# Kernel optimization log

Measured on AMD Instinct MI355X. Metric: run time of the kernel, lower is better.

Reference implementation:

```python
import jax, jax.numpy as jnp
import numpy as np

N_NODES = 100000
N_EDGES = 1600000
IN_DIM = 48
HID = 128
BN_EPS = 1e-5


def _batchnorm(h, gamma, beta):
    # BatchNorm1d in training mode: batch mean, biased variance
    mu = jnp.mean(h, axis=0)
    var = jnp.mean(jnp.square(h - mu), axis=0)
    return (h - mu) * jax.lax.rsqrt(var + BN_EPS) * gamma + beta


def setup_inputs() -> dict:
    key = jax.random.key(0)
    ks = jax.random.split(key, 8)
    x = jax.random.normal(ks[0], (N_NODES, IN_DIM), dtype=jnp.float32)
    edge_index = jax.random.randint(ks[1], (2, N_EDGES), 0, N_NODES, dtype=jnp.int64)
    s1 = 1.0 / np.sqrt(IN_DIM)
    s2 = 1.0 / np.sqrt(HID)
    return {
        "x": x,
        "edge_index": edge_index,
        "W1": jax.random.uniform(ks[2], (HID, IN_DIM), jnp.float32, -s1, s1),
        "b1": jnp.zeros((HID,), jnp.float32),
        "g1": jnp.ones((HID,), jnp.float32),
        "be1": jnp.zeros((HID,), jnp.float32),
        "Wl": jax.random.uniform(ks[3], (HID, HID), jnp.float32, -s2, s2),
        "bl": jnp.zeros((HID,), jnp.float32),
        "Wr": jax.random.uniform(ks[4], (HID, HID), jnp.float32, -s2, s2),
        "g2": jnp.ones((HID,), jnp.float32),
        "be2": jnp.zeros((HID,), jnp.float32),
    }


def reference(x, edge_index, W1, b1, g1, be1, Wl, bl, Wr, g2, be2):
    # input projection: Linear -> BatchNorm -> ReLU
    h = x @ W1.T + b1                               # [N, HID]
    feat = jax.nn.relu(_batchnorm(h, g1, be1))      # [N, HID]

    # SAGEConv (mean aggregation): messages flow src -> dst
    src, dst = edge_index[0], edge_index[1]
    summed = jax.ops.segment_sum(feat[src], dst, num_segments=N_NODES)  # [N, HID]
    cnt = jax.ops.segment_sum(jnp.ones((N_EDGES,), jnp.float32), dst, num_segments=N_NODES)
    agg = summed / jnp.maximum(cnt, 1.0)[:, None]
    sage = agg @ Wl.T + bl + feat @ Wr.T            # lin_l(mean) + lin_r(self)

    out_feat = _batchnorm(sage, g2, be2)
    return (feat, out_feat)
```

## Files before the change

kernel.cpp:

```cpp
#include <hip/hip_runtime.h>
#include <hip/hip_bf16.h>

#define NN 100000
#define NE 1600000
#define INDIM 48
#define HID 128
#define K2 256
#define KP 64
#define BN_EPS 1e-5f

#define NBUK 782
#define BCAP 2816
#define CHUNK 8192
#define NBB 196
#define NPB 16

#define MT ((NN + 63) / 64)
#define MT2 ((NN + 127) / 128)

typedef short s8v __attribute__((ext_vector_type(8)));
typedef float f4v __attribute__((ext_vector_type(4)));
typedef float f2v __attribute__((ext_vector_type(2)));

__device__ __forceinline__ unsigned short f2bf(float f) {
    __hip_bfloat16 b = __float2bfloat16(f);
    unsigned short u;
    __builtin_memcpy(&u, &b, 2);
    return u;
}
__device__ __forceinline__ float bflo(unsigned u) { return __uint_as_float(u << 16); }
__device__ __forceinline__ float bfhi(unsigned u) { return __uint_as_float(u & 0xffff0000u); }
__device__ __forceinline__ unsigned packbf(float lo, float hi) {
    return (unsigned)f2bf(lo) | ((unsigned)f2bf(hi) << 16);
}

__global__ __launch_bounds__(512) void k_bucket_prep(const int* __restrict__ ei,
                                                     int* __restrict__ bcur,
                                                     unsigned int* __restrict__ bbuf,
                                                     const float* __restrict__ Wl,
                                                     const float* __restrict__ Wr,
                                                     const float* __restrict__ W1,
                                                     unsigned short* __restrict__ Wcat,
                                                     unsigned short* __restrict__ W1b) {
  int tid = threadIdx.x;
  if (blockIdx.x >= NBB) {
    int t0 = (blockIdx.x - NBB) * 512 + tid;
    for (int i = t0; i < HID * K2; i += NPB * 512) {
      int j = i >> 8, k = i & (K2 - 1);
      float v = (k < HID) ? Wl[j * HID + k] : Wr[j * HID + (k - HID)];
      Wcat[i] = f2bf(v);
    }
    for (int i = t0; i < HID * KP; i += NPB * 512) {
      int j = i >> 6, k = i & (KP - 1);
      W1b[i] = (k < INDIM) ? f2bf(W1[j * INDIM + k]) : (unsigned short)0;
    }
    return;
  }
  __shared__ int cnt[1024];
  __shared__ int sc[2][1024];
  __shared__ int ofs[1024];
  __shared__ int lcur[1024];
  __shared__ int gbase[1024];
  __shared__ unsigned int stag[CHUNK];
  __shared__ unsigned short sbkt[CHUNK];
  int base = blockIdx.x * CHUNK;
  int lim = min(CHUNK, NE - base);
  cnt[tid] = 0;
  cnt[tid + 512] = 0;
  __syncthreads();
#pragma unroll
  for (int i = 0; i < CHUNK / 512; ++i) {
    int e = i * 512 + tid;
    if (e < lim) {
      int d = ei[NE + base + e];
      d = min(max(d, 0), NN - 1);
      atomicAdd(&cnt[d >> 7], 1);
    }
  }
  __syncthreads();
  sc[0][tid] = cnt[tid];
  sc[0][tid + 512] = cnt[tid + 512];
  __syncthreads();
  int pp = 0;
  for (int d = 1; d < 1024; d <<= 1) {
    int a0 = sc[pp][tid];
    int a1 = sc[pp][tid + 512];
    if (tid >= d) a0 += sc[pp][tid - d];
    a1 += sc[pp][tid + 512 - d];
    sc[pp ^ 1][tid] = a0;
    sc[pp ^ 1][tid + 512] = a1;
    __syncthreads();
    pp ^= 1;
  }
  ofs[tid] = sc[pp][tid] - cnt[tid];
  ofs[tid + 512] = sc[pp][tid + 512] - cnt[tid + 512];
  lcur[tid] = ofs[tid];
  lcur[tid + 512] = ofs[tid + 512];
  if (tid < NBUK) gbase[tid] = atomicAdd(&bcur[tid], cnt[tid]);
  if (tid + 512 < NBUK) gbase[tid + 512] = atomicAdd(&bcur[tid + 512], cnt[tid + 512]);
  __syncthreads();
#pragma unroll
  for (int i = 0; i < CHUNK / 512; ++i) {
    int e = i * 512 + tid;
    if (e < lim) {
      int s = ei[base + e];
      int d = ei[NE + base + e];
      s = min(max(s, 0), NN - 1);
      d = min(max(d, 0), NN - 1);
      int b = d >> 7;
      int pos = atomicAdd(&lcur[b], 1);
      stag[pos] = (unsigned)s | ((unsigned)(d & 127) << 17);
      sbkt[pos] = (unsigned short)b;
    }
  }
  __syncthreads();
  for (int s = tid; s < lim; s += 512) {
    int b = sbkt[s];
    int off = gbase[b] + (s - ofs[b]);
    if (off < BCAP) bbuf[(size_t)b * BCAP + off] = stag[s];
  }
}

__global__ __launch_bounds__(256) void k_proj_gemm(
    const float* __restrict__ x, const unsigned short* __restrict__ W1b,
    const float* __restrict__ b1, unsigned short* __restrict__ Abuf,
    float* __restrict__ colSum, float* __restrict__ colSq) {
  __shared__ __align__(16) unsigned short Bsh[HID][KP + 8];
  __shared__ float redS[4][HID], redQ[4][HID];
  int tid = threadIdx.x;
  for (int i = tid; i < HID * (KP / 8); i += 256) {
    int j = i >> 3, kg = (i & 7) << 3;
    *(s8v*)&Bsh[j][kg] = *(const s8v*)(W1b + (size_t)j * KP + kg);
  }
  __syncthreads();
  int w = tid >> 6, l = tid & 63;
  int m16 = l & 15, q = l >> 4;
  float bcol[8];
#pragma unroll
  for (int nt = 0; nt < 8; ++nt) bcol[nt] = b1[nt * 16 + m16];
  float ssum[8], ssq[8];
#pragma unroll
  for (int nt = 0; nt < 8; ++nt) { ssum[nt] = 0.f; ssq[nt] = 0.f; }
  f4v zero4 = {0.f, 0.f, 0.f, 0.f};
  s8v zero8 = {0, 0, 0, 0, 0, 0, 0, 0};
  for (int tile = blockIdx.x; tile < MT; tile += gridDim.x) {
    int row = tile * 64 + w * 16 + m16;
    bool rv = row < NN;
    const float* xr = x + (size_t)row * INDIM;
    f4v acc[8];
#pragma unroll
    for (int nt = 0; nt < 8; ++nt) acc[nt] = zero4;
#pragma unroll
    for (int kt = 0; kt < 2; ++kt) {
      int c0 = kt * 32 + q * 8;
      s8v a = zero8;
      if (rv && c0 < INDIM) {
        float4 v0 = *(const float4*)(xr + c0);
        float4 v1 = *(const float4*)(xr + c0 + 4);
        a[0] = (short)f2bf(v0.x); a[1] = (short)f2bf(v0.y);
        a[2] = (short)f2bf(v0.z); a[3] = (short)f2bf(v0.w);
        a[4] = (short)f2bf(v1.x); a[5] = (short)f2bf(v1.y);
        a[6] = (short)f2bf(v1.z); a[7] = (short)f2bf(v1.w);
      }
#pragma unroll
      for (int nt = 0; nt < 8; ++nt) {
        s8v b = *(const s8v*)(&Bsh[nt * 16 + m16][kt * 32 + q * 8]);
        acc[nt] = __builtin_amdgcn_mfma_f32_16x16x32_bf16(a, b, acc[nt], 0, 0, 0);
      }
    }
    int rbase = tile * 64 + w * 16 + q * 4;
#pragma unroll
    for (int nt = 0; nt < 8; ++nt) {
      int col = nt * 16 + m16;
#pragma unroll
      for (int r4 = 0; r4 < 4; ++r4) {
        int rr = rbase + r4;
        if (rr < NN) {
          float v = acc[nt][r4] + bcol[nt];
          Abuf[(size_t)rr * K2 + HID + col] = f2bf(v);
          ssum[nt] += v;
          ssq[nt] = fmaf(v, v, ssq[nt]);
        }
      }
    }
  }
#pragma unroll
  for (int nt = 0; nt < 8; ++nt) {
    float s = ssum[nt], qq = ssq[nt];
    s += __shfl_xor(s, 16);
    s += __shfl_xor(s, 32);
    qq += __shfl_xor(qq, 16);
    qq += __shfl_xor(qq, 32);
    if (q == 0) {
      redS[w][nt * 16 + m16] = s;
      redQ[w][nt * 16 + m16] = qq;
    }
  }
  __syncthreads();
  if (tid < HID) {
    float s = redS[0][tid] + redS[1][tid] + redS[2][tid] + redS[3][tid];
    float qq = redQ[0][tid] + redQ[1][tid] + redQ[2][tid] + redQ[3][tid];
    atomicAdd(&colSum[tid], s);
    atomicAdd(&colSq[tid], qq);
  }
}

__global__ __launch_bounds__(256) void k_apply(float* __restrict__ feat,
                                               const float* __restrict__ colSum,
                                               const float* __restrict__ colSq,
                                               const float* __restrict__ g1,
                                               const float* __restrict__ be1,
                                               unsigned short* __restrict__ A,
                                               unsigned char* __restrict__ feat8) {
  __shared__ __align__(16) float sa[HID], sb[HID];
  int tid = threadIdx.x;
  if (tid < HID) {
    float mu = colSum[tid] * (1.0f / NN);
    float var = fmaxf(colSq[tid] * (1.0f / NN) - mu * mu, 0.f);
    float a = g1[tid] * rsqrtf(var + BN_EPS);
    sa[tid] = a;
    sb[tid] = be1[tid] - mu * a;
  }
  __syncthreads();
  int i = blockIdx.x * 256 + tid;
  if (i >= NN * 16) return;
  int r = i >> 4, c8 = (i & 15) << 3;
  unsigned short* ap = A + (size_t)r * K2 + HID + c8;
  uint4 hv = *(const uint4*)ap;
  float4 a0 = *(const float4*)(sa + c8);
  float4 a1 = *(const float4*)(sa + c8 + 4);
  float4 b0 = *(const float4*)(sb + c8);
  float4 b1 = *(const float4*)(sb + c8 + 4);
  float f0 = fmaxf(fmaf(bflo(hv.x), a0.x, b0.x), 0.f);
  float f1 = fmaxf(fmaf(bfhi(hv.x), a0.y, b0.y), 0.f);
  float f2 = fmaxf(fmaf(bflo(hv.y), a0.z, b0.z), 0.f);
  float f3 = fmaxf(fmaf(bfhi(hv.y), a0.w, b0.w), 0.f);
  float f4 = fmaxf(fmaf(bflo(hv.z), a1.x, b1.x), 0.f);
  float f5 = fmaxf(fmaf(bfhi(hv.z), a1.y, b1.y), 0.f);
  float f6 = fmaxf(fmaf(bflo(hv.w), a1.z, b1.z), 0.f);
  float f7 = fmaxf(fmaf(bfhi(hv.w), a1.w, b1.w), 0.f);
  float4 o0 = {f0, f1, f2, f3}, o1 = {f4, f5, f6, f7};
  *(float4*)(feat + (size_t)r * HID + c8) = o0;
  *(float4*)(feat + (size_t)r * HID + c8 + 4) = o1;
  uint4 ob;
  ob.x = packbf(f0, f1);
  ob.y = packbf(f2, f3);
  ob.z = packbf(f4, f5);
  ob.w = packbf(f6, f7);
  *(uint4*)ap = ob;
  unsigned p0 = __builtin_amdgcn_cvt_pk_fp8_f32(f0, f1, 0u, false);
  p0 = __builtin_amdgcn_cvt_pk_fp8_f32(f2, f3, p0, true);
  unsigned p1 = __builtin_amdgcn_cvt_pk_fp8_f32(f4, f5, 0u, false);
  p1 = __builtin_amdgcn_cvt_pk_fp8_f32(f6, f7, p1, true);
  uint2 o8 = {p0, p1};
  *(uint2*)(feat8 + (size_t)r * HID + c8) = o8;
}

__global__ __launch_bounds__(512) void k_bucket_agg(const unsigned int* __restrict__ bbuf,
                                                    const int* __restrict__ bcnt,
                                                    const unsigned char* __restrict__ feat8,
                                                    unsigned short* __restrict__ Abuf) {
  __shared__ unsigned int lcsr[BCAP];
  __shared__ int cnt[128], ofs[128], cur[128];
  __shared__ int sc[2][128];
  int tid = threadIdx.x;
  int b = blockIdx.x;
  int m = min(bcnt[b], BCAP);
  int n0 = b << 7;
  int nb = min(128, NN - n0);
  if (tid < 128) cnt[tid] = 0;
  __syncthreads();
  const unsigned int* bp = bbuf + (size_t)b * BCAP;
  for (int s = tid; s < m; s += 512) {
    unsigned p = bp[s];
    atomicAdd(&cnt[(p >> 17) & 127], 1);
  }
  __syncthreads();
  if (tid < 128) sc[0][tid] = cnt[tid];
  __syncthreads();
  int pp = 0;
  for (int d = 1; d < 128; d <<= 1) {
    if (tid < 128) {
      int v = sc[pp][tid];
      if (tid >= d) v += sc[pp][tid - d];
      sc[pp ^ 1][tid] = v;
    }
    __syncthreads();
    pp ^= 1;
  }
  if (tid < 128) {
    int o = sc[pp][tid] - cnt[tid];
    ofs[tid] = o;
    cur[tid] = o;
  }
  __syncthreads();
  for (int s = tid; s < m; s += 512) {
    unsigned p = bp[s];
    int ld = (p >> 17) & 127;
    int pos = atomicAdd(&cur[ld], 1);
    lcsr[pos] = p & 0x1FFFF;
  }
  __syncthreads();
  int lane = tid & 31;
  int g = tid >> 5;
  int half = (lane >> 3) & 3;
  int l8 = lane & 7;
  for (int ln = g; ln < nb; ln += 16) {
    int deg = cnt[ln], beg = ofs[ln];
    float ac[16];
#pragma unroll
    for (int i = 0; i < 16; ++i) ac[i] = 0.f;
#pragma unroll 2
    for (int j = 0; j < deg; j += 4) {
      int idx = j + half;
      uint4 v = {0u, 0u, 0u, 0u};
      if (idx < deg) {
        int s = lcsr[beg + idx];
        v = *(const uint4*)(feat8 + (size_t)s * HID + l8 * 16);
      }
      f2v d;
      d = __builtin_amdgcn_cvt_pk_f32_fp8(v.x, false); ac[0] += d.x;  ac[1] += d.y;
      d = __builtin_amdgcn_cvt_pk_f32_fp8(v.x, true);  ac[2] += d.x;  ac[3] += d.y;
      d = __builtin_amdgcn_cvt_pk_f32_fp8(v.y, false); ac[4] += d.x;  ac[5] += d.y;
      d = __builtin_amdgcn_cvt_pk_f32_fp8(v.y, true);  ac[6] += d.x;  ac[7] += d.y;
      d = __builtin_amdgcn_cvt_pk_f32_fp8(v.z, false); ac[8] += d.x;  ac[9] += d.y;
      d = __builtin_amdgcn_cvt_pk_f32_fp8(v.z, true);  ac[10] += d.x; ac[11] += d.y;
      d = __builtin_amdgcn_cvt_pk_f32_fp8(v.w, false); ac[12] += d.x; ac[13] += d.y;
      d = __builtin_amdgcn_cvt_pk_f32_fp8(v.w, true);  ac[14] += d.x; ac[15] += d.y;
    }
#pragma unroll
    for (int i = 0; i < 16; ++i) {
      ac[i] += __shfl_xor(ac[i], 8);
      ac[i] += __shfl_xor(ac[i], 16);
    }
    if (half == 0) {
      float inv = 1.f / fmaxf((float)deg, 1.f);
      uint4 o0, o1;
      o0.x = packbf(ac[0] * inv, ac[1] * inv);
      o0.y = packbf(ac[2] * inv, ac[3] * inv);
      o0.z = packbf(ac[4] * inv, ac[5] * inv);
      o0.w = packbf(ac[6] * inv, ac[7] * inv);
      o1.x = packbf(ac[8] * inv, ac[9] * inv);
      o1.y = packbf(ac[10] * inv, ac[11] * inv);
      o1.z = packbf(ac[12] * inv, ac[13] * inv);
      o1.w = packbf(ac[14] * inv, ac[15] * inv);
      unsigned short* op = Abuf + (size_t)(n0 + ln) * K2 + l8 * 16;
      *(uint4*)op = o0;
      *(uint4*)(op + 8) = o1;
    }
  }
}

__global__ __launch_bounds__(512) void k_gemm(
    const unsigned short* __restrict__ A, const unsigned short* __restrict__ Wcat,
    const float* __restrict__ bl, unsigned short* __restrict__ sageb,
    float* __restrict__ colSum, float* __restrict__ colSq) {
  __shared__ __align__(16) unsigned short Bsh[HID][264];
  __shared__ float redS[8][HID], redQ[8][HID];
  int tid = threadIdx.x;
  for (int i = tid; i < HID * 32; i += 512) {
    int j = i >> 5;
    int kg = (i & 31) << 3;
    *(s8v*)&Bsh[j][kg] = *(const s8v*)(Wcat + (size_t)j * K2 + kg);
  }
  __syncthreads();
  int w = tid >> 6, l = tid & 63;
  int m16 = l & 15, q = l >> 4;
  int tile = blockIdx.x;
  int row = tile * 128 + w * 16 + m16;
  bool rv = row < NN;
  f4v zero4 = {0.f, 0.f, 0.f, 0.f};
  s8v zero8 = {0, 0, 0, 0, 0, 0, 0, 0};
  f4v acc[8];
#pragma unroll
  for (int nt = 0; nt < 8; ++nt) acc[nt] = zero4;
#pragma unroll
  for (int kt = 0; kt < 8; ++kt) {
    s8v a = zero8;
    if (rv) a = *(const s8v*)(A + (size_t)row * K2 + kt * 32 + q * 8);
#pragma unroll
    for (int nt = 0; nt < 8; ++nt) {
      s8v bfr = *(const s8v*)(&Bsh[nt * 16 + m16][kt * 32 + q * 8]);
      acc[nt] = __builtin_amdgcn_mfma_f32_16x16x32_bf16(a, bfr, acc[nt], 0, 0, 0);
    }
  }
  int rbase = tile * 128 + w * 16 + q * 4;
  float ssum[8], ssq[8];
#pragma unroll
  for (int nt = 0; nt < 8; ++nt) { ssum[nt] = 0.f; ssq[nt] = 0.f; }
#pragma unroll
  for (int nt = 0; nt < 8; ++nt) {
    int col = nt * 16 + m16;
    float bv = bl[col];
#pragma unroll
    for (int r4 = 0; r4 < 4; ++r4) {
      int rr = rbase + r4;
      if (rr < NN) {
        float v = acc[nt][r4] + bv;
        sageb[(size_t)rr * HID + col] = f2bf(v);
        ssum[nt] += v;
        ssq[nt] = fmaf(v, v, ssq[nt]);
      }
    }
  }
#pragma unroll
  for (int nt = 0; nt < 8; ++nt) {
    float s = ssum[nt], qq = ssq[nt];
    s += __shfl_xor(s, 16);
    s += __shfl_xor(s, 32);
    qq += __shfl_xor(qq, 16);
    qq += __shfl_xor(qq, 32);
    if (q == 0) {
      redS[w][nt * 16 + m16] = s;
      redQ[w][nt * 16 + m16] = qq;
    }
  }
  __syncthreads();
  if (tid < HID) {
    float s = 0.f, qq = 0.f;
#pragma unroll
    for (int ww = 0; ww < 8; ++ww) { s += redS[ww][tid]; qq += redQ[ww][tid]; }
    atomicAdd(&colSum[tid], s);
    atomicAdd(&colSq[tid], qq);
  }
}

__global__ __launch_bounds__(256) void k_bn_apply(const unsigned short* __restrict__ sageb,
                                                  float* __restrict__ out,
                                                  const float* __restrict__ colSum,
                                                  const float* __restrict__ colSq,
                                                  const float* __restrict__ g2,
                                                  const float* __restrict__ be2) {
  __shared__ __align__(16) float sa[HID], sb[HID];
  int tid = threadIdx.x;
  if (tid < HID) {
    float mu = colSum[tid] * (1.0f / NN);
    float var = fmaxf(colSq[tid] * (1.0f / NN) - mu * mu, 0.f);
    float a = g2[tid] * rsqrtf(var + BN_EPS);
    sa[tid] = a;
    sb[tid] = be2[tid] - mu * a;
  }
  __syncthreads();
  int i = blockIdx.x * 256 + tid;
  if (i >= NN * 16) return;
  int r = i >> 4, c8 = (i & 15) << 3;
  uint4 sv = *(const uint4*)(sageb + (size_t)r * HID + c8);
  float4 a0 = *(const float4*)(sa + c8);
  float4 a1 = *(const float4*)(sa + c8 + 4);
  float4 b0 = *(const float4*)(sb + c8);
  float4 b1 = *(const float4*)(sb + c8 + 4);
  float4 o0, o1;
  o0.x = fmaf(bflo(sv.x), a0.x, b0.x);
  o0.y = fmaf(bfhi(sv.x), a0.y, b0.y);
  o0.z = fmaf(bflo(sv.y), a0.z, b0.z);
  o0.w = fmaf(bfhi(sv.y), a0.w, b0.w);
  o1.x = fmaf(bflo(sv.z), a1.x, b1.x);
  o1.y = fmaf(bfhi(sv.z), a1.y, b1.y);
  o1.z = fmaf(bflo(sv.w), a1.z, b1.z);
  o1.w = fmaf(bfhi(sv.w), a1.w, b1.w);
  *(float4*)(out + (size_t)r * HID + c8) = o0;
  *(float4*)(out + (size_t)r * HID + c8 + 4) = o1;
}

extern "C" void kernel_launch(void* const* d_in, const int* in_sizes, int n_in,
                              void* d_out, int out_size, void* d_ws, size_t ws_size,
                              hipStream_t stream) {
  const float* x   = (const float*)d_in[0];
  const int*   ei  = (const int*)d_in[1];
  const float* W1  = (const float*)d_in[2];
  const float* b1  = (const float*)d_in[3];
  const float* g1  = (const float*)d_in[4];
  const float* be1 = (const float*)d_in[5];
  const float* Wl  = (const float*)d_in[6];
  const float* bl  = (const float*)d_in[7];
  const float* Wr  = (const float*)d_in[8];
  const float* g2  = (const float*)d_in[9];
  const float* be2 = (const float*)d_in[10];

  float* feat_out = (float*)d_out;
  float* out2     = (float*)d_out + (size_t)NN * HID;

  size_t off = 0;
  auto alloc = [&](size_t bytes) -> void* {
    void* p = (char*)d_ws + off;
    off += (bytes + 255) & ~(size_t)255;
    return p;
  };
  float*          stats = (float*)alloc(4 * HID * 4);
  int*            bcur  = (int*)alloc((size_t)NBUK * 4);
  unsigned short* Abuf  = (unsigned short*)alloc((size_t)NN * K2 * 2);
  unsigned char*  feat8 = (unsigned char*)alloc((size_t)NN * HID);
  unsigned short* sageb = (unsigned short*)alloc((size_t)NN * HID * 2);
  unsigned int*   bbuf  = (unsigned int*)alloc((size_t)NBUK * BCAP * 4);
  unsigned short* Wcat  = (unsigned short*)alloc((size_t)HID * K2 * 2);
  unsigned short* W1b   = (unsigned short*)alloc((size_t)HID * KP * 2);
  float* colSum1 = stats;
  float* colSq1  = stats + HID;
  float* colSum2 = stats + 2 * HID;
  float* colSq2  = stats + 3 * HID;

  hipMemsetAsync(stats, 0, 4 * HID * 4 + (size_t)NBUK * 4, stream);
  k_bucket_prep<<<NBB + NPB, 512, 0, stream>>>(ei, bcur, bbuf, Wl, Wr, W1, Wcat, W1b);
  k_proj_gemm<<<512, 256, 0, stream>>>(x, W1b, b1, Abuf, colSum1, colSq1);
  k_apply<<<(NN * 16 + 255) / 256, 256, 0, stream>>>(feat_out, colSum1, colSq1, g1, be1, Abuf, feat8);
  k_bucket_agg<<<NBUK, 512, 0, stream>>>(bbuf, bcur, feat8, Abuf);
  k_gemm<<<MT2, 512, 0, stream>>>(Abuf, Wcat, bl, sageb, colSum2, colSq2);
  k_bn_apply<<<(NN * 16 + 255) / 256, 256, 0, stream>>>(sageb, out2, colSum2, colSq2, g2, be2);
}
```

Baseline: 289.5 us.

## Fuse bucket prep with input projection and GEMM with BN via grid barrier

Merges the edge bucketing kernel and the input projection GEMM into one launch, with the two paths sharing a union of shared-memory layouts. Weight conversion to bf16 moves into the GEMM kernels that use it. The final SAGE GEMM now keeps two row tiles per block in registers, waits on a global atomic spin barrier for the column statistics, and writes the normalized output directly. This removes the bf16 sage intermediate buffer and the separate BN-apply pass. It relies on all 391 blocks being co-resident, which is not guaranteed; the spin has a timeout that would yield wrong statistics if it fires.

```diff
diff --git a/kernel.cpp b/kernel.cpp
--- a/kernel.cpp
+++ b/kernel.cpp
@@ -13,10 +13,10 @@
 #define BCAP 2816
 #define CHUNK 8192
 #define NBB 196
-#define NPB 16
-
-#define MT ((NN + 63) / 64)
+#define NPRJ 320
+
 #define MT2 ((NN + 127) / 128)
+#define GF (MT2 / 2)
 
 typedef short s8v __attribute__((ext_vector_type(8)));
 typedef float f4v __attribute__((ext_vector_type(4)));
@@ -34,103 +34,98 @@
     return (unsigned)f2bf(lo) | ((unsigned)f2bf(hi) << 16);
 }
 
-__global__ __launch_bounds__(512) void k_bucket_prep(const int* __restrict__ ei,
-                                                     int* __restrict__ bcur,
-                                                     unsigned int* __restrict__ bbuf,
-                                                     const float* __restrict__ Wl,
-                                                     const float* __restrict__ Wr,
-                                                     const float* __restrict__ W1,
-                                                     unsigned short* __restrict__ Wcat,
-                                                     unsigned short* __restrict__ W1b) {
+__global__ __launch_bounds__(512) void k_prep_proj(const int* __restrict__ ei,
+                                                   int* __restrict__ bcur,
+                                                   unsigned int* __restrict__ bbuf,
+                                                   const float* __restrict__ x,
+                                                   const float* __restrict__ W1,
+                                                   const float* __restrict__ b1,
+                                                   unsigned short* __restrict__ Abuf,
+                                                   float* __restrict__ colSum,
+                                                   float* __restrict__ colSq) {
+  union __align__(16) SMem {
+    struct {
+      int cnt[1024];
+      int sc[2][1024];
+      int ofs[1024];
+      int lcur[1024];
+      int gbase[1024];
+      unsigned int stag[CHUNK];
+      unsigned short sbkt[CHUNK];
+    } p;
+    struct {
+      unsigned short Bsh[HID][KP + 8];
+      float redS[8][HID];
+      float redQ[8][HID];
+    } g;
+  };
+  __shared__ SMem sm;
   int tid = threadIdx.x;
-  if (blockIdx.x >= NBB) {
-    int t0 = (blockIdx.x - NBB) * 512 + tid;
-    for (int i = t0; i < HID * K2; i += NPB * 512) {
-      int j = i >> 8, k = i & (K2 - 1);
-      float v = (k < HID) ? Wl[j * HID + k] : Wr[j * HID + (k - HID)];
-      Wcat[i] = f2bf(v);
-    }
-    for (int i = t0; i < HID * KP; i += NPB * 512) {
-      int j = i >> 6, k = i & (KP - 1);
-      W1b[i] = (k < INDIM) ? f2bf(W1[j * INDIM + k]) : (unsigned short)0;
+
+  if (blockIdx.x < NBB) {
+    int base = blockIdx.x * CHUNK;
+    int lim = min(CHUNK, NE - base);
+    sm.p.cnt[tid] = 0;
+    sm.p.cnt[tid + 512] = 0;
+    __syncthreads();
+#pragma unroll
+    for (int i = 0; i < CHUNK / 512; ++i) {
+      int e = i * 512 + tid;
+      if (e < lim) {
+        int d = ei[NE + base + e];
+        d = min(max(d, 0), NN - 1);
+        atomicAdd(&sm.p.cnt[d >> 7], 1);
+      }
+    }
+    __syncthreads();
+    sm.p.sc[0][tid] = sm.p.cnt[tid];
+    sm.p.sc[0][tid + 512] = sm.p.cnt[tid + 512];
+    __syncthreads();
+    int pp = 0;
+    for (int d = 1; d < 1024; d <<= 1) {
+      int a0 = sm.p.sc[pp][tid];
+      int a1 = sm.p.sc[pp][tid + 512];
+      if (tid >= d) a0 += sm.p.sc[pp][tid - d];
+      a1 += sm.p.sc[pp][tid + 512 - d];
+      sm.p.sc[pp ^ 1][tid] = a0;
+      sm.p.sc[pp ^ 1][tid + 512] = a1;
+      __syncthreads();
+      pp ^= 1;
+    }
+    sm.p.ofs[tid] = sm.p.sc[pp][tid] - sm.p.cnt[tid];
+    sm.p.ofs[tid + 512] = sm.p.sc[pp][tid + 512] - sm.p.cnt[tid + 512];
+    sm.p.lcur[tid] = sm.p.ofs[tid];
+    sm.p.lcur[tid + 512] = sm.p.ofs[tid + 512];
+    if (tid < NBUK) sm.p.gbase[tid] = atomicAdd(&bcur[tid], sm.p.cnt[tid]);
+    if (tid + 512 < NBUK) sm.p.gbase[tid + 512] = atomicAdd(&bcur[tid + 512], sm.p.cnt[tid + 512]);
+    __syncthreads();
+#pragma unroll
+    for (int i = 0; i < CHUNK / 512; ++i) {
+      int e = i * 512 + tid;
+      if (e < lim) {
+        int s = ei[base + e];
+        int d = ei[NE + base + e];
+        s = min(max(s, 0), NN - 1);
+        d = min(max(d, 0), NN - 1);
+        int b = d >> 7;
+        int pos = atomicAdd(&sm.p.lcur[b], 1);
+        sm.p.stag[pos] = (unsigned)s | ((unsigned)(d & 127) << 17);
+        sm.p.sbkt[pos] = (unsigned short)b;
+      }
+    }
+    __syncthreads();
+    for (int s = tid; s < lim; s += 512) {
+      int b = sm.p.sbkt[s];
+      int off = sm.p.gbase[b] + (s - sm.p.ofs[b]);
+      if (off < BCAP) bbuf[(size_t)b * BCAP + off] = sm.p.stag[s];
     }
     return;
   }
-  __shared__ int cnt[1024];
-  __shared__ int sc[2][1024];
-  __shared__ int ofs[1024];
-  __shared__ int lcur[1024];
-  __shared__ int gbase[1024];
-  __shared__ unsigned int stag[CHUNK];
-  __shared__ unsigned short sbkt[CHUNK];
-  int base = blockIdx.x * CHUNK;
-  int lim = min(CHUNK, NE - base);
-  cnt[tid] = 0;
-  cnt[tid + 512] = 0;
-  __syncthreads();
-#pragma unroll
-  for (int i = 0; i < CHUNK / 512; ++i) {
-    int e = i * 512 + tid;
-    if (e < lim) {
-      int d = ei[NE + base + e];
-      d = min(max(d, 0), NN - 1);
-      atomicAdd(&cnt[d >> 7], 1);
-    }
-  }
-  __syncthreads();
-  sc[0][tid] = cnt[tid];
-  sc[0][tid + 512] = cnt[tid + 512];
-  __syncthreads();
-  int pp = 0;
-  for (int d = 1; d < 1024; d <<= 1) {
-    int a0 = sc[pp][tid];
-    int a1 = sc[pp][tid + 512];
-    if (tid >= d) a0 += sc[pp][tid - d];
-    a1 += sc[pp][tid + 512 - d];
-    sc[pp ^ 1][tid] = a0;
-    sc[pp ^ 1][tid + 512] = a1;
-    __syncthreads();
-    pp ^= 1;
-  }
-  ofs[tid] = sc[pp][tid] - cnt[tid];
-  ofs[tid + 512] = sc[pp][tid + 512] - cnt[tid + 512];
-  lcur[tid] = ofs[tid];
-  lcur[tid + 512] = ofs[tid + 512];
-  if (tid < NBUK) gbase[tid] = atomicAdd(&bcur[tid], cnt[tid]);
-  if (tid + 512 < NBUK) gbase[tid + 512] = atomicAdd(&bcur[tid + 512], cnt[tid + 512]);
-  __syncthreads();
-#pragma unroll
-  for (int i = 0; i < CHUNK / 512; ++i) {
-    int e = i * 512 + tid;
-    if (e < lim) {
-      int s = ei[base + e];
-      int d = ei[NE + base + e];
-      s = min(max(s, 0), NN - 1);
-      d = min(max(d, 0), NN - 1);
-      int b = d >> 7;
-      int pos = atomicAdd(&lcur[b], 1);
-      stag[pos] = (unsigned)s | ((unsigned)(d & 127) << 17);
-      sbkt[pos] = (unsigned short)b;
-    }
-  }
-  __syncthreads();
-  for (int s = tid; s < lim; s += 512) {
-    int b = sbkt[s];
-    int off = gbase[b] + (s - ofs[b]);
-    if (off < BCAP) bbuf[(size_t)b * BCAP + off] = stag[s];
-  }
-}
-
-__global__ __launch_bounds__(256) void k_proj_gemm(
-    const float* __restrict__ x, const unsigned short* __restrict__ W1b,
-    const float* __restrict__ b1, unsigned short* __restrict__ Abuf,
-    float* __restrict__ colSum, float* __restrict__ colSq) {
-  __shared__ __align__(16) unsigned short Bsh[HID][KP + 8];
-  __shared__ float redS[4][HID], redQ[4][HID];
-  int tid = threadIdx.x;
-  for (int i = tid; i < HID * (KP / 8); i += 256) {
-    int j = i >> 3, kg = (i & 7) << 3;
-    *(s8v*)&Bsh[j][kg] = *(const s8v*)(W1b + (size_t)j * KP + kg);
+
+  int bid2 = blockIdx.x - NBB;
+  for (int i = tid; i < HID * KP; i += 512) {
+    int j = i >> 6, k = i & (KP - 1);
+    sm.g.Bsh[j][k] = (k < INDIM) ? f2bf(W1[j * INDIM + k]) : (unsigned short)0;
   }
   __syncthreads();
   int w = tid >> 6, l = tid & 63;
@@ -143,8 +138,8 @@
   for (int nt = 0; nt < 8; ++nt) { ssum[nt] = 0.f; ssq[nt] = 0.f; }
   f4v zero4 = {0.f, 0.f, 0.f, 0.f};
   s8v zero8 = {0, 0, 0, 0, 0, 0, 0, 0};
-  for (int tile = blockIdx.x; tile < MT; tile += gridDim.x) {
-    int row = tile * 64 + w * 16 + m16;
+  for (int tile = bid2; tile < MT2; tile += NPRJ) {
+    int row = tile * 128 + w * 16 + m16;
     bool rv = row < NN;
     const float* xr = x + (size_t)row * INDIM;
     f4v acc[8];
@@ -164,11 +159,11 @@
       }
 #pragma unroll
       for (int nt = 0; nt < 8; ++nt) {
-        s8v b = *(const s8v*)(&Bsh[nt * 16 + m16][kt * 32 + q * 8]);
+        s8v b = *(const s8v*)(&sm.g.Bsh[nt * 16 + m16][kt * 32 + q * 8]);
         acc[nt] = __builtin_amdgcn_mfma_f32_16x16x32_bf16(a, b, acc[nt], 0, 0, 0);
       }
     }
-    int rbase = tile * 64 + w * 16 + q * 4;
+    int rbase = tile * 128 + w * 16 + q * 4;
 #pragma unroll
     for (int nt = 0; nt < 8; ++nt) {
       int col = nt * 16 + m16;
@@ -192,14 +187,15 @@
     qq += __shfl_xor(qq, 16);
     qq += __shfl_xor(qq, 32);
     if (q == 0) {
-      redS[w][nt * 16 + m16] = s;
-      redQ[w][nt * 16 + m16] = qq;
+      sm.g.redS[w][nt * 16 + m16] = s;
+      sm.g.redQ[w][nt * 16 + m16] = qq;
     }
   }
   __syncthreads();
   if (tid < HID) {
-    float s = redS[0][tid] + redS[1][tid] + redS[2][tid] + redS[3][tid];
-    float qq = redQ[0][tid] + redQ[1][tid] + redQ[2][tid] + redQ[3][tid];
+    float s = 0.f, qq = 0.f;
+#pragma unroll
+    for (int ww = 0; ww < 8; ++ww) { s += sm.g.redS[ww][tid]; qq += sm.g.redQ[ww][tid]; }
     atomicAdd(&colSum[tid], s);
     atomicAdd(&colSq[tid], qq);
   }
@@ -351,55 +347,68 @@
   }
 }
 
-__global__ __launch_bounds__(512) void k_gemm(
-    const unsigned short* __restrict__ A, const unsigned short* __restrict__ Wcat,
-    const float* __restrict__ bl, unsigned short* __restrict__ sageb,
-    float* __restrict__ colSum, float* __restrict__ colSq) {
+__global__ __launch_bounds__(512, 4) void k_gemm_fused(
+    const unsigned short* __restrict__ A,
+    const float* __restrict__ Wl, const float* __restrict__ Wr,
+    const float* __restrict__ bl, const float* __restrict__ g2, const float* __restrict__ be2,
+    float* __restrict__ out2, float* __restrict__ colSum, float* __restrict__ colSq,
+    int* __restrict__ abar) {
   __shared__ __align__(16) unsigned short Bsh[HID][264];
   __shared__ float redS[8][HID], redQ[8][HID];
+  __shared__ float sa[HID], sb[HID];
   int tid = threadIdx.x;
-  for (int i = tid; i < HID * 32; i += 512) {
-    int j = i >> 5;
-    int kg = (i & 31) << 3;
-    *(s8v*)&Bsh[j][kg] = *(const s8v*)(Wcat + (size_t)j * K2 + kg);
+  for (int i4 = tid; i4 < HID * K2 / 4; i4 += 512) {
+    int i = i4 << 2;
+    int j = i >> 8, k = i & (K2 - 1);
+    const float* src = (k < HID) ? (Wl + j * HID + k) : (Wr + j * HID + (k - HID));
+    float4 v = *(const float4*)src;
+    uint2 u;
+    u.x = packbf(v.x, v.y);
+    u.y = packbf(v.z, v.w);
+    *(uint2*)&Bsh[j][k] = u;
   }
   __syncthreads();
   int w = tid >> 6, l = tid & 63;
   int m16 = l & 15, q = l >> 4;
-  int tile = blockIdx.x;
-  int row = tile * 128 + w * 16 + m16;
-  bool rv = row < NN;
+  float bcol[8];
+#pragma unroll
+  for (int nt = 0; nt < 8; ++nt) bcol[nt] = bl[nt * 16 + m16];
   f4v zero4 = {0.f, 0.f, 0.f, 0.f};
   s8v zero8 = {0, 0, 0, 0, 0, 0, 0, 0};
-  f4v acc[8];
-#pragma unroll
-  for (int nt = 0; nt < 8; ++nt) acc[nt] = zero4;
-#pragma unroll
-  for (int kt = 0; kt < 8; ++kt) {
-    s8v a = zero8;
-    if (rv) a = *(const s8v*)(A + (size_t)row * K2 + kt * 32 + q * 8);
+  f4v acc[2][8];
+#pragma unroll
+  for (int t = 0; t < 2; ++t) {
+    int tile = blockIdx.x * 2 + t;
+    int row = tile * 128 + w * 16 + m16;
+    bool rv = row < NN;
+#pragma unroll
+    for (int nt = 0; nt < 8; ++nt) acc[t][nt] = zero4;
+#pragma unroll
+    for (int kt = 0; kt < 8; ++kt) {
+      s8v a = zero8;
+      if (rv) a = *(const s8v*)(A + (size_t)row * K2 + kt * 32 + q * 8);
+#pragma unroll
+      for (int nt = 0; nt < 8; ++nt) {
+        s8v bfr = *(const s8v*)(&Bsh[nt * 16 + m16][kt * 32 + q * 8]);
+        acc[t][nt] = __builtin_amdgcn_mfma_f32_16x16x32_bf16(a, bfr, acc[t][nt], 0, 0, 0);
+      }
+    }
+  }
+  float ssum[8], ssq[8];
+#pragma unroll
+  for (int nt = 0; nt < 8; ++nt) { ssum[nt] = 0.f; ssq[nt] = 0.f; }
+#pragma unroll
+  for (int t = 0; t < 2; ++t) {
+    int rbase = (blockIdx.x * 2 + t) * 128 + w * 16 + q * 4;
 #pragma unroll
     for (int nt = 0; nt < 8; ++nt) {
-      s8v bfr = *(const s8v*)(&Bsh[nt * 16 + m16][kt * 32 + q * 8]);
-      acc[nt] = __builtin_amdgcn_mfma_f32_16x16x32_bf16(a, bfr, acc[nt], 0, 0, 0);
-    }
-  }
-  int rbase = tile * 128 + w * 16 + q * 4;
-  float ssum[8], ssq[8];
-#pragma unroll
-  for (int nt = 0; nt < 8; ++nt) { ssum[nt] = 0.f; ssq[nt] = 0.f; }
-#pragma unroll
-  for (int nt = 0; nt < 8; ++nt) {
-    int col = nt * 16 + m16;
-    float bv = bl[col];
-#pragma unroll
-    for (int r4 = 0; r4 < 4; ++r4) {
-      int rr = rbase + r4;
-      if (rr < NN) {
-        float v = acc[nt][r4] + bv;
-        sageb[(size_t)rr * HID + col] = f2bf(v);
-        ssum[nt] += v;
-        ssq[nt] = fmaf(v, v, ssq[nt]);
+#pragma unroll
+      for (int r4 = 0; r4 < 4; ++r4) {
+        if (rbase + r4 < NN) {
+          float v = acc[t][nt][r4] + bcol[nt];
+          ssum[nt] += v;
+          ssq[nt] = fmaf(v, v, ssq[nt]);
+        }
       }
     }
   }
@@ -423,43 +432,40 @@
     atomicAdd(&colSum[tid], s);
     atomicAdd(&colSq[tid], qq);
   }
-}
-
-__global__ __launch_bounds__(256) void k_bn_apply(const unsigned short* __restrict__ sageb,
-                                                  float* __restrict__ out,
-                                                  const float* __restrict__ colSum,
-                                                  const float* __restrict__ colSq,
-                                                  const float* __restrict__ g2,
-                                                  const float* __restrict__ be2) {
-  __shared__ __align__(16) float sa[HID], sb[HID];
-  int tid = threadIdx.x;
+  __syncthreads();
+  if (tid == 0) {
+    __hip_atomic_fetch_add(abar, 1, __ATOMIC_RELEASE, __HIP_MEMORY_SCOPE_AGENT);
+    int spin = 0;
+    while (__hip_atomic_load(abar, __ATOMIC_ACQUIRE, __HIP_MEMORY_SCOPE_AGENT) < GF) {
+      __builtin_amdgcn_s_sleep(8);
+      if (++spin > 4000000) break;
+    }
+  }
+  __syncthreads();
   if (tid < HID) {
-    float mu = colSum[tid] * (1.0f / NN);
-    float var = fmaxf(colSq[tid] * (1.0f / NN) - mu * mu, 0.f);
+    float s  = __hip_atomic_load(&colSum[tid], __ATOMIC_RELAXED, __HIP_MEMORY_SCOPE_AGENT);
+    float qq = __hip_atomic_load(&colSq[tid],  __ATOMIC_RELAXED, __HIP_MEMORY_SCOPE_AGENT);
+    float mu = s * (1.0f / NN);
+    float var = fmaxf(qq * (1.0f / NN) - mu * mu, 0.f);
     float a = g2[tid] * rsqrtf(var + BN_EPS);
     sa[tid] = a;
     sb[tid] = be2[tid] - mu * a;
   }
   __syncthreads();
-  int i = blockIdx.x * 256 + tid;
-  if (i >= NN * 16) return;
-  int r = i >> 4, c8 = (i & 15) << 3;
-  uint4 sv = *(const uint4*)(sageb + (size_t)r * HID + c8);
-  float4 a0 = *(const float4*)(sa + c8);
-  float4 a1 = *(const float4*)(sa + c8 + 4);
-  float4 b0 = *(const float4*)(sb + c8);
-  float4 b1 = *(const float4*)(sb + c8 + 4);
-  float4 o0, o1;
-  o0.x = fmaf(bflo(sv.x), a0.x, b0.x);
-  o0.y = fmaf(bfhi(sv.x), a0.y, b0.y);
-  o0.z = fmaf(bflo(sv.y), a0.z, b0.z);
-  o0.w = fmaf(bfhi(sv.y), a0.w, b0.w);
-  o1.x = fmaf(bflo(sv.z), a1.x, b1.x);
-  o1.y = fmaf(bfhi(sv.z), a1.y, b1.y);
-  o1.z = fmaf(bflo(sv.w), a1.z, b1.z);
-  o1.w = fmaf(bfhi(sv.w), a1.w, b1.w);
-  *(float4*)(out + (size_t)r * HID + c8) = o0;
-  *(float4*)(out + (size_t)r * HID + c8 + 4) = o1;
+#pragma unroll
+  for (int t = 0; t < 2; ++t) {
+    int rbase = (blockIdx.x * 2 + t) * 128 + w * 16 + q * 4;
+#pragma unroll
+    for (int nt = 0; nt < 8; ++nt) {
+      int col = nt * 16 + m16;
+      float a_ = sa[col], b_ = sb[col];
+#pragma unroll
+      for (int r4 = 0; r4 < 4; ++r4) {
+        int rr = rbase + r4;
+        if (rr < NN) out2[(size_t)rr * HID + col] = fmaf(acc[t][nt][r4] + bcol[nt], a_, b_);
+      }
+    }
+  }
 }
 
 extern "C" void kernel_launch(void* const* d_in, const int* in_sizes, int n_in,
@@ -486,24 +492,20 @@
     off += (bytes + 255) & ~(size_t)255;
     return p;
   };
-  float*          stats = (float*)alloc(4 * HID * 4);
+  float*          stats = (float*)alloc(4 * HID * 4 + 256);
   int*            bcur  = (int*)alloc((size_t)NBUK * 4);
   unsigned short* Abuf  = (unsigned short*)alloc((size_t)NN * K2 * 2);
   unsigned char*  feat8 = (unsigned char*)alloc((size_t)NN * HID);
-  unsigned short* sageb = (unsigned short*)alloc((size_t)NN * HID * 2);
   unsigned int*   bbuf  = (unsigned int*)alloc((size_t)NBUK * BCAP * 4);
-  unsigned short* Wcat  = (unsigned short*)alloc((size_t)HID * K2 * 2);
-  unsigned short* W1b   = (unsigned short*)alloc((size_t)HID * KP * 2);
   float* colSum1 = stats;
   float* colSq1  = stats + HID;
   float* colSum2 = stats + 2 * HID;
   float* colSq2  = stats + 3 * HID;
-
-  hipMemsetAsync(stats, 0, 4 * HID * 4 + (size_t)NBUK * 4, stream);
-  k_bucket_prep<<<NBB + NPB, 512, 0, stream>>>(ei, bcur, bbuf, Wl, Wr, W1, Wcat, W1b);
-  k_proj_gemm<<<512, 256, 0, stream>>>(x, W1b, b1, Abuf, colSum1, colSq1);
+  int*   abar    = (int*)(stats + 4 * HID);
+
+  hipMemsetAsync(stats, 0, 4 * HID * 4 + 256 + (size_t)NBUK * 4, stream);
+  k_prep_proj<<<NBB + NPRJ, 512, 0, stream>>>(ei, bcur, bbuf, x, W1, b1, Abuf, colSum1, colSq1);
   k_apply<<<(NN * 16 + 255) / 256, 256, 0, stream>>>(feat_out, colSum1, colSq1, g1, be1, Abuf, feat8);
   k_bucket_agg<<<NBUK, 512, 0, stream>>>(bbuf, bcur, feat8, Abuf);
-  k_gemm<<<MT2, 512, 0, stream>>>(Abuf, Wcat, bl, sageb, colSum2, colSq2);
-  k_bn_apply<<<(NN * 16 + 255) / 256, 256, 0, stream>>>(sageb, out2, colSum2, colSq2, g2, be2);
-}
+  k_gemm_fused<<<GF, 512, 0, stream>>>(Abuf, Wl, Wr, bl, g2, be2, out2, colSum2, colSq2, abar);
+}
```

Result: slower. 422.5 us (+45.9%).
